# Kernel optimization log

Measured on AMD Instinct MI355X. Metric: run time of the kernel, lower is better.

Reference implementation:

```python
import jax, jax.numpy as jnp
import numpy as np

D, H, HD, FF, L, SYM, B = 256, 8, 32, 256, 3, 64, 32768


def setup_inputs() -> dict:
    key = jax.random.key(0)
    ks = iter(jax.random.split(key, 32))
    n = lambda shape, s=0.02: jax.random.normal(next(ks), shape, dtype=jnp.float32) * s
    return {
        "global_emb": n((B, D), 1.0),
        "pert_emb": n((B, D), 1.0),
        "sym_feat": n((B, SYM), 1.0),
        "ppi_feat": n((B, D), 1.0),
        "sym_W": n((SYM, D)),
        "sym_b": jnp.zeros((D,), jnp.float32),
        "sym_ln_g": jnp.ones((D,), jnp.float32),
        "sym_ln_b": jnp.zeros((D,), jnp.float32),
        "token_type_emb": n((4, D)),
        "Wqkv": n((L, D, 3 * D)),
        "bqkv": jnp.zeros((L, 3 * D), jnp.float32),
        "Wo": n((L, D, D)),
        "bo": jnp.zeros((L, D), jnp.float32),
        "ln1_g": jnp.ones((L, D), jnp.float32),
        "ln1_b": jnp.zeros((L, D), jnp.float32),
        "ln2_g": jnp.ones((L, D), jnp.float32),
        "ln2_b": jnp.zeros((L, D), jnp.float32),
        "W1": n((L, D, FF)),
        "b1": jnp.zeros((L, FF), jnp.float32),
        "W2": n((L, FF, D)),
        "b2": jnp.zeros((L, D), jnp.float32),
        "final_ln_g": jnp.ones((D,), jnp.float32),
        "final_ln_b": jnp.zeros((D,), jnp.float32),
        "out_ln_g": jnp.ones((D,), jnp.float32),
        "out_ln_b": jnp.zeros((D,), jnp.float32),
    }


def _ln(x, g, b, eps=1e-5):
    m = jnp.mean(x, axis=-1, keepdims=True)
    v = jnp.mean(jnp.square(x - m), axis=-1, keepdims=True)
    return (x - m) * jax.lax.rsqrt(v + eps) * g + b


def reference(global_emb, pert_emb, sym_feat, ppi_feat, sym_W, sym_b, sym_ln_g,
              sym_ln_b, token_type_emb, Wqkv, bqkv, Wo, bo, ln1_g, ln1_b,
              ln2_g, ln2_b, W1, b1, W2, b2, final_ln_g, final_ln_b,
              out_ln_g, out_ln_b):
    # sym projection + LN, then stack 4 tokens and add token-type embedding
    sym_proj = _ln(sym_feat @ sym_W + sym_b, sym_ln_g, sym_ln_b)
    x = jnp.stack([global_emb, pert_emb, sym_proj, ppi_feat], axis=1)  # [B,4,D]
    x = x + token_type_emb[None]
    Bsz = x.shape[0]
    scale = 1.0 / np.sqrt(HD).astype(np.float32)
    for l in range(L):  # pre-norm TransformerEncoderLayer x3 (eval: dropout off)
        h = _ln(x, ln1_g[l], ln1_b[l])
        qkv = h @ Wqkv[l] + bqkv[l]  # [B,4,3D]
        q, k, v = jnp.split(qkv, 3, axis=-1)
        q = q.reshape(Bsz, 4, H, HD).transpose(0, 2, 1, 3)  # [B,H,4,HD]
        k = k.reshape(Bsz, 4, H, HD).transpose(0, 2, 1, 3)
        v = v.reshape(Bsz, 4, H, HD).transpose(0, 2, 1, 3)
        attn = jax.nn.softmax(jnp.einsum("bhqd,bhkd->bhqk", q, k) * scale, axis=-1)
        o = jnp.einsum("bhqk,bhkd->bhqd", attn, v)
        o = o.transpose(0, 2, 1, 3).reshape(Bsz, 4, D)
        x = x + (o @ Wo[l] + bo[l])
        h2 = _ln(x, ln2_g[l], ln2_b[l])
        ff = jax.nn.gelu(h2 @ W1[l] + b1[l], approximate=False) @ W2[l] + b2[l]
        x = x + ff
    x = _ln(x, final_ln_g, final_ln_b)  # TransformerEncoder final norm
    return _ln(jnp.mean(x, axis=1), out_ln_g, out_ln_b)  # mean over 4 tokens + out_norm
```

## Files before the change

kernel.cpp:

```cpp
#include <hip/hip_runtime.h>
#include <hip/hip_bf16.h>
#include <math.h>

typedef unsigned short u16;
typedef __attribute__((ext_vector_type(8))) short v8s;
typedef __attribute__((ext_vector_type(4))) short v4s;
typedef __attribute__((ext_vector_type(4))) float v4f;

__device__ __forceinline__ float bf2f(u16 u){
  union { float f; unsigned int i; } v; v.i = ((unsigned int)u) << 16; return v.f;
}
__device__ __forceinline__ u16 f2bf(float f){
  union { __hip_bfloat16 h; u16 u; } cv; cv.h = __float2bfloat16(f); return cv.u;
}
__device__ __forceinline__ bool det_bf16(const void* p){
  return ((const u16*)p)[0] != 0;
}
__device__ __forceinline__ float ldp(const void* p, size_t i, bool bf){
  return bf ? bf2f(((const u16*)p)[i]) : ((const float*)p)[i];
}
__device__ __forceinline__ void ld8f(const void* p, size_t i, bool bf, float* o){
  if (bf){
    v8s a = *(const v8s*)((const u16*)p + i);
    #pragma unroll
    for (int j=0;j<8;j++) o[j]=bf2f((u16)a[j]);
  } else {
    const float4* q=(const float4*)((const float*)p + i);
    float4 a=q[0], b=q[1];
    o[0]=a.x;o[1]=a.y;o[2]=a.z;o[3]=a.w;o[4]=b.x;o[5]=b.y;o[6]=b.z;o[7]=b.w;
  }
}
__device__ __forceinline__ void ld4f(const void* p, size_t i, bool bf, float* o){
  if (bf){
    v4s a = *(const v4s*)((const u16*)p + i);
    #pragma unroll
    for (int j=0;j<4;j++) o[j]=bf2f((u16)a[j]);
  } else {
    float4 q = *(const float4*)((const float*)p + i);
    o[0]=q.x;o[1]=q.y;o[2]=q.z;o[3]=q.w;
  }
}

#define MFMA(a,b,c) __builtin_amdgcn_mfma_f32_16x16x32_bf16((a),(b),(c),0,0,0)

template<int CTRL>
__device__ __forceinline__ float dpp_qp(float x){
  union { float f; int i; } u; u.f = x;
  u.i = __builtin_amdgcn_mov_dpp(u.i, CTRL, 0xF, 0xF, true);
  return u.f;
}

__device__ __forceinline__ int swz(int row, int col, int stride){
  return row*stride + ((((col>>3) ^ (row&7))<<3) | (col&7));
}

__device__ __forceinline__ void st4(u16* dst, v4f a, const float* b){
  v4s o;
  #pragma unroll
  for (int i=0;i<4;i++) o[i] = (short)f2bf(a[i] + b[i]);
  *(v4s*)dst = o;
}
__device__ __forceinline__ void rmw4(u16* p, v4f a, const float* b){
  v4s x = *(v4s*)p; v4s o;
  #pragma unroll
  for (int i=0;i<4;i++) o[i] = (short)f2bf(bf2f((u16)x[i]) + a[i] + b[i]);
  *(v4s*)p = o;
}

__device__ __forceinline__ float gelu_f(float u){
  float ax = fabsf(u)*0.70710678118f;
  float t = 1.f/(1.f + 0.3275911f*ax);
  float y = t*(0.254829592f + t*(-0.284496736f + t*(1.421413741f +
            t*(-1.453152027f + t*1.061405429f))));
  float er = 1.f - y*__expf(-ax*ax);
  er = copysignf(er, u);
  return 0.5f*u*(1.f + er);
}

__global__ __launch_bounds__(64) void repack_kernel(
    const void* __restrict__ symW, const void* __restrict__ Wqkv,
    const void* __restrict__ Wo, const void* __restrict__ W1, const void* __restrict__ W2,
    u16* __restrict__ wf_sym, u16* __restrict__ wf_qkv, u16* __restrict__ wf_o,
    u16* __restrict__ wf_1, u16* __restrict__ wf_2, const void* __restrict__ dtp)
{
  bool bf = det_bf16(dtp);
  int idx = blockIdx.x;
  const void* src; u16* dst; int N, kb, nb; size_t soff;
  if (idx < 32) { src = symW; dst = wf_sym; N = 256; kb = idx >> 4; nb = idx & 15; soff = 0; }
  else {
    idx -= 32;
    int lay = idx / 768, r = idx % 768;
    if (r < 384) { N = 768; src = Wqkv; soff = (size_t)lay*196608; dst = wf_qkv + lay*196608; kb = r/48; nb = r%48; }
    else {
      r -= 384; int which = r >> 7, rr = r & 127; N = 256; kb = rr >> 4; nb = rr & 15;
      soff = (size_t)lay*65536;
      if (which == 0)      { src = Wo; dst = wf_o + lay*65536; }
      else if (which == 1) { src = W1; dst = wf_1 + lay*65536; }
      else                 { src = W2; dst = wf_2 + lay*65536; }
    }
  }
  int ln = threadIdx.x;
  int n  = nb*16 + (ln & 15);
  int k0 = kb*32 + (ln >> 4)*8;
  u16* d = dst + (((size_t)(kb*(N>>4) + nb))*64 + ln)*8;
  #pragma unroll
  for (int j = 0; j < 8; j++) d[j] = f2bf(ldp(src, soff + (size_t)(k0+j)*N + n, bf));
}

__device__ __forceinline__ void ln64s(const u16* src, u16* dst,
    const void* gp, const void* bp, size_t goff, bool bf, int t)
{
  int r = t>>3, p = t&7;
  float vv[32];
  float su=0.f, sq=0.f;
  #pragma unroll
  for (int k4=0;k4<4;k4++){
    v8s a = *(const v8s*)(src + swz(r, p*32+k4*8, 256));
    #pragma unroll
    for (int j=0;j<8;j++){ float v=bf2f((u16)a[j]); vv[k4*8+j]=v; su+=v; sq+=v*v; }
  }
  su += dpp_qp<0xB1>(su); sq += dpp_qp<0xB1>(sq);
  su += dpp_qp<0x4E>(su); sq += dpp_qp<0x4E>(sq);
  su += __shfl_xor(su,4); sq += __shfl_xor(sq,4);
  float m = su*(1.f/256.f);
  float rs = rsqrtf(sq*(1.f/256.f) - m*m + 1e-5f);
  #pragma unroll
  for (int k4=0;k4<4;k4++){
    float gg[8], bb[8];
    ld8f(gp, goff + p*32 + k4*8, bf, gg);
    ld8f(bp, goff + p*32 + k4*8, bf, bb);
    v8s o;
    #pragma unroll
    for (int j=0;j<8;j++) o[j]=(short)f2bf((vv[k4*8+j]-m)*rs*gg[j]+bb[j]);
    *(v8s*)(dst + swz(r, p*32+k4*8, 256)) = o;
  }
}

__global__ __launch_bounds__(512,4) void fused_kernel(
    const void* __restrict__ gemb, const void* __restrict__ pemb,
    const void* __restrict__ symf, const void* __restrict__ ppi,
    const void* __restrict__ symb, const void* __restrict__ slng,
    const void* __restrict__ slnb, const void* __restrict__ tte,
    const void* __restrict__ bqkv, const void* __restrict__ bo,
    const void* __restrict__ ln1g, const void* __restrict__ ln1b,
    const void* __restrict__ ln2g, const void* __restrict__ ln2b,
    const void* __restrict__ b1p, const void* __restrict__ b2p,
    const void* __restrict__ flng, const void* __restrict__ flnb,
    const void* __restrict__ olng, const void* __restrict__ olnb,
    const u16* __restrict__ wf_sym, const u16* __restrict__ wf_qkv,
    const u16* __restrict__ wf_o, const u16* __restrict__ wf_1,
    const u16* __restrict__ wf_2,
    void* __restrict__ out)
{
  __shared__ __align__(16) u16 X[16384];
  __shared__ __align__(16) u16 H[16384];
  __shared__ __align__(16) u16 symst[1024];

  bool bf = det_bf16(slng);
  int t = threadIdx.x;
  int w = t>>6, ln = t&63, quad = ln>>4, c = ln&15;
  int row0 = blockIdx.x * 64;
  int S0 = row0 >> 2;

  {
    if (t < 128){
      int r = t>>3, pp = t&7;
      float tmp[8];
      ld8f(symf, (size_t)(S0+r)*64 + pp*8, bf, tmp);
      v8s o;
      #pragma unroll
      for (int j=0;j<8;j++) o[j]=(short)f2bf(tmp[j]);
      *(v8s*)(symst + swz(r, pp*8, 64)) = o;
    } else {
      int u = t-128;
      int rid = u>>3, p = u&7;
      int s = rid/3, z = rid - s*3;
      int tok = (z==2)?3:z;
      const void* src = (z==0)?gemb: (z==1)?pemb: ppi;
      #pragma unroll
      for (int k4=0;k4<4;k4++){
        float a8[8], t8[8];
        ld8f(src, (size_t)(S0+s)*256 + p*32 + k4*8, bf, a8);
        ld8f(tte, (size_t)tok*256 + p*32 + k4*8, bf, t8);
        v8s o;
        #pragma unroll
        for (int j=0;j<8;j++) o[j]=(short)f2bf(a8[j]+t8[j]);
        *(v8s*)(X + swz(s*4+tok, p*32+k4*8, 256)) = o;
      }
    }
    __syncthreads();
    {
      v4f acc[2];
      v4f z4={0.f,0.f,0.f,0.f};
      acc[0]=z4; acc[1]=z4;
      #pragma unroll
      for (int kb=0;kb<2;kb++){
        v8s a = *(const v8s*)(symst + swz(c, kb*32+quad*8, 64));
        #pragma unroll
        for (int j=0;j<2;j++){
          v8s b = *(const v8s*)(wf_sym + (((size_t)(kb*16+w*2+j))*64+ln)*8);
          acc[j] = MFMA(b, a, acc[j]);
        }
      }
      #pragma unroll
      for (int j=0;j<2;j++){
        int colb = (w*2+j)*16 + quad*4;
        float sb[4]; ld4f(symb, colb, bf, sb);
        st4(H + swz(c, colb, 256), acc[j], sb);
      }
    }
    __syncthreads();
    if (t < 128){
      int r = t>>3, p = t&7;
      float vv[32];
      float su=0.f, sq=0.f;
      #pragma unroll
      for (int k4=0;k4<4;k4++){
        v8s a = *(const v8s*)(H + swz(r, p*32+k4*8, 256));
        #pragma unroll
        for (int j=0;j<8;j++){ float v=bf2f((u16)a[j]); vv[k4*8+j]=v; su+=v; sq+=v*v; }
      }
      su += dpp_qp<0xB1>(su); sq += dpp_qp<0xB1>(sq);
      su += dpp_qp<0x4E>(su); sq += dpp_qp<0x4E>(sq);
      su += __shfl_xor(su,4); sq += __shfl_xor(sq,4);
      float m = su*(1.f/256.f);
      float rs = rsqrtf(sq*(1.f/256.f) - m*m + 1e-5f);
      #pragma unroll
      for (int k4=0;k4<4;k4++){
        float gg[8], bb[8], t8[8];
        ld8f(slng, p*32+k4*8, bf, gg);
        ld8f(slnb, p*32+k4*8, bf, bb);
        ld8f(tte, 512 + p*32+k4*8, bf, t8);
        v8s o;
        #pragma unroll
        for (int j=0;j<8;j++) o[j]=(short)f2bf((vv[k4*8+j]-m)*rs*gg[j]+bb[j]+t8[j]);
        *(v8s*)(X + swz(r*4+2, p*32+k4*8, 256)) = o;
      }
    }
    __syncthreads();
  }

  #pragma unroll 1
  for (int lay = 0; lay < 3; lay++){

    ln64s(X, H, ln1g, ln1b, (size_t)lay*256, bf, t);
    __syncthreads();

    {
      const u16* wq = wf_qkv + (size_t)lay*196608;
      int h = w;
      v4f z4={0.f,0.f,0.f,0.f};
      const float scl = 0.17677669529663687f;
      v4f p01[2], p23[2];
      auto qkhalf = [&](int hf, v4f* pout){
        v4f Qa[2][2], Ka[2][2];
        #pragma unroll
        for (int m2=0;m2<2;m2++){ Qa[m2][0]=z4;Qa[m2][1]=z4;Ka[m2][0]=z4;Ka[m2][1]=z4; }
        #pragma unroll 2
        for (int kb=0;kb<8;kb++){
          v8s Bq0 = *(const v8s*)(wq + (((size_t)(kb*48      + h*2  ))*64+ln)*8);
          v8s Bq1 = *(const v8s*)(wq + (((size_t)(kb*48      + h*2+1))*64+ln)*8);
          v8s Bk0 = *(const v8s*)(wq + (((size_t)(kb*48 + 16 + h*2  ))*64+ln)*8);
          v8s Bk1 = *(const v8s*)(wq + (((size_t)(kb*48 + 16 + h*2+1))*64+ln)*8);
          #pragma unroll
          for (int m2=0;m2<2;m2++){
            v8s a = *(const v8s*)(H + swz((hf*2+m2)*16+c, kb*32+quad*8, 256));
            Qa[m2][0]=MFMA(Bq0,a,Qa[m2][0]);
            Qa[m2][1]=MFMA(Bq1,a,Qa[m2][1]);
            Ka[m2][0]=MFMA(Bk0,a,Ka[m2][0]);
            Ka[m2][1]=MFMA(Bk1,a,Ka[m2][1]);
          }
        }
        float bq2[2][4], bk2[2][4];
        #pragma unroll
        for (int jj=0;jj<2;jj++){
          ld4f(bqkv, (size_t)lay*768 +       h*32 + jj*16 + quad*4, bf, bq2[jj]);
          ld4f(bqkv, (size_t)lay*768 + 256 + h*32 + jj*16 + quad*4, bf, bk2[jj]);
        }
        #pragma unroll
        for (int m2=0;m2<2;m2++){
          float q8[8], k8[8];
          #pragma unroll
          for (int jj=0;jj<2;jj++)
            #pragma unroll
            for (int i=0;i<4;i++){
              q8[jj*4+i] = Qa[m2][jj][i] + bq2[jj][i];
              k8[jj*4+i] = Ka[m2][jj][i] + bk2[jj][i];
            }
          float sp0=0.f, sp1=0.f, sp2=0.f, sp3=0.f;
          #pragma unroll
          for (int x=0;x<8;x++){
            sp0 += q8[x]*k8[x];
            sp1 += q8[x]*dpp_qp<0xB1>(k8[x]);
            sp2 += q8[x]*dpp_qp<0x4E>(k8[x]);
            sp3 += q8[x]*dpp_qp<0x1B>(k8[x]);
          }
          sp0 += __shfl_xor(sp0,16); sp0 += __shfl_xor(sp0,32);
          sp1 += __shfl_xor(sp1,16); sp1 += __shfl_xor(sp1,32);
          sp2 += __shfl_xor(sp2,16); sp2 += __shfl_xor(sp2,32);
          sp3 += __shfl_xor(sp3,16); sp3 += __shfl_xor(sp3,32);
          float s0=sp0*scl, s1=sp1*scl, s2=sp2*scl, s3=sp3*scl;
          float mx = fmaxf(fmaxf(s0,s1),fmaxf(s2,s3));
          float e0=__expf(s0-mx), e1=__expf(s1-mx), e2=__expf(s2-mx), e3=__expf(s3-mx);
          float inv = 1.f/(e0+e1+e2+e3);
          v4f p; p[0]=e0*inv; p[1]=e1*inv; p[2]=e2*inv; p[3]=e3*inv;
          pout[m2] = p;
        }
      };
      qkhalf(0, p01);
      __builtin_amdgcn_sched_barrier(0);
      qkhalf(1, p23);
      v4f Va[4][2];
      #pragma unroll
      for (int mb=0;mb<4;mb++){ Va[mb][0]=z4; Va[mb][1]=z4; }
      #pragma unroll 2
      for (int kb=0;kb<8;kb++){
        v8s Bv0 = *(const v8s*)(wq + (((size_t)(kb*48 + 32 + h*2  ))*64+ln)*8);
        v8s Bv1 = *(const v8s*)(wq + (((size_t)(kb*48 + 32 + h*2+1))*64+ln)*8);
        #pragma unroll
        for (int mb=0;mb<4;mb++){
          v8s a = *(const v8s*)(H + swz(mb*16+c, kb*32+quad*8, 256));
          Va[mb][0]=MFMA(Bv0,a,Va[mb][0]);
          Va[mb][1]=MFMA(Bv1,a,Va[mb][1]);
        }
      }
      __syncthreads();
      float bv[2][4];
      #pragma unroll
      for (int jj=0;jj<2;jj++)
        ld4f(bqkv, (size_t)lay*768 + 512 + h*32 + jj*16 + quad*4, bf, bv[jj]);
      #pragma unroll
      for (int mb=0;mb<4;mb++){
        v4f P = (mb==0)?p01[0]:(mb==1)?p01[1]:(mb==2)?p23[0]:p23[1];
        #pragma unroll
        for (int jj=0;jj<2;jj++){
          v4f o;
          #pragma unroll
          for (int i=0;i<4;i++){
            float v = Va[mb][jj][i] + bv[jj][i];
            float r = P[0]*v;
            r += P[1]*dpp_qp<0xB1>(v);
            r += P[2]*dpp_qp<0x4E>(v);
            r += P[3]*dpp_qp<0x1B>(v);
            o[i] = r;
          }
          v4s pk;
          #pragma unroll
          for (int i=0;i<4;i++) pk[i]=(short)f2bf(o[i]);
          *(v4s*)(H + swz(mb*16+c, h*32 + jj*16 + quad*4, 256)) = pk;
        }
      }
    }
    __syncthreads();

    {
      const u16* wo = wf_o + (size_t)lay*65536;
      v4f acc[4][2];
      v4f z4={0.f,0.f,0.f,0.f};
      #pragma unroll
      for (int mb=0;mb<4;mb++){ acc[mb][0]=z4; acc[mb][1]=z4; }
      #pragma unroll 2
      for (int kb=0;kb<8;kb++){
        v8s B0 = *(const v8s*)(wo + (((size_t)(kb*16 + w*2  ))*64+ln)*8);
        v8s B1 = *(const v8s*)(wo + (((size_t)(kb*16 + w*2+1))*64+ln)*8);
        #pragma unroll
        for (int mb=0;mb<4;mb++){
          v8s a = *(const v8s*)(H + swz(mb*16+c, kb*32+quad*8, 256));
          acc[mb][0]=MFMA(B0,a,acc[mb][0]);
          acc[mb][1]=MFMA(B1,a,acc[mb][1]);
        }
      }
      #pragma unroll
      for (int jj=0;jj<2;jj++){
        int colb = (w*2+jj)*16 + quad*4;
        float bs[4]; ld4f(bo, (size_t)lay*256 + colb, bf, bs);
        #pragma unroll
        for (int mb=0;mb<4;mb++)
          rmw4(X + swz(mb*16+c, colb, 256), acc[mb][jj], bs);
      }
    }
    __syncthreads();

    ln64s(X, H, ln2g, ln2b, (size_t)lay*256, bf, t);
    __syncthreads();

    {
      const u16* w1 = wf_1 + (size_t)lay*65536;
      v4f acc[4][2];
      v4f z4={0.f,0.f,0.f,0.f};
      #pragma unroll
      for (int mb=0;mb<4;mb++){ acc[mb][0]=z4; acc[mb][1]=z4; }
      #pragma unroll 2
      for (int kb=0;kb<8;kb++){
        v8s B0 = *(const v8s*)(w1 + (((size_t)(kb*16 + w*2  ))*64+ln)*8);
        v8s B1 = *(const v8s*)(w1 + (((size_t)(kb*16 + w*2+1))*64+ln)*8);
        #pragma unroll
        for (int mb=0;mb<4;mb++){
          v8s a = *(const v8s*)(H + swz(mb*16+c, kb*32+quad*8, 256));
          acc[mb][0]=MFMA(B0,a,acc[mb][0]);
          acc[mb][1]=MFMA(B1,a,acc[mb][1]);
        }
      }
      __syncthreads();
      #pragma unroll
      for (int jj=0;jj<2;jj++){
        int colb = (w*2+jj)*16 + quad*4;
        float bs[4]; ld4f(b1p, (size_t)lay*256 + colb, bf, bs);
        #pragma unroll
        for (int mb=0;mb<4;mb++){
          v4s pk;
          #pragma unroll
          for (int i=0;i<4;i++) pk[i]=(short)f2bf(gelu_f(acc[mb][jj][i] + bs[i]));
          *(v4s*)(H + swz(mb*16+c, colb, 256)) = pk;
        }
      }
    }
    __syncthreads();

    {
      const u16* w2 = wf_2 + (size_t)lay*65536;
      v4f acc[4][2];
      v4f z4={0.f,0.f,0.f,0.f};
      #pragma unroll
      for (int mb=0;mb<4;mb++){ acc[mb][0]=z4; acc[mb][1]=z4; }
      #pragma unroll 2
      for (int kb=0;kb<8;kb++){
        v8s B0 = *(const v8s*)(w2 + (((size_t)(kb*16 + w*2  ))*64+ln)*8);
        v8s B1 = *(const v8s*)(w2 + (((size_t)(kb*16 + w*2+1))*64+ln)*8);
        #pragma unroll
        for (int mb=0;mb<4;mb++){
          v8s a = *(const v8s*)(H + swz(mb*16+c, kb*32+quad*8, 256));
          acc[mb][0]=MFMA(B0,a,acc[mb][0]);
          acc[mb][1]=MFMA(B1,a,acc[mb][1]);
        }
      }
      #pragma unroll
      for (int jj=0;jj<2;jj++){
        int colb = (w*2+jj)*16 + quad*4;
        float bs[4]; ld4f(b2p, (size_t)lay*256 + colb, bf, bs);
        #pragma unroll
        for (int mb=0;mb<4;mb++)
          rmw4(X + swz(mb*16+c, colb, 256), acc[mb][jj], bs);
      }
    }
    __syncthreads();
  }

  ln64s(X, H, flng, flnb, 0, bf, t);
  __syncthreads();
  if (t < 128){
    int s = t>>3, p = t&7;
    float y[32];
    #pragma unroll
    for (int j=0;j<32;j++) y[j]=0.f;
    #pragma unroll
    for (int r4=0;r4<4;r4++)
      #pragma unroll
      for (int k4=0;k4<4;k4++){
        v8s a = *(const v8s*)(H + swz(s*4+r4, p*32+k4*8, 256));
        #pragma unroll
        for (int j=0;j<8;j++) y[k4*8+j] += bf2f((u16)a[j]);
      }
    float su=0.f, sq=0.f;
    #pragma unroll
    for (int j=0;j<32;j++){ y[j]*=0.25f; su+=y[j]; sq+=y[j]*y[j]; }
    su += dpp_qp<0xB1>(su); sq += dpp_qp<0xB1>(sq);
    su += dpp_qp<0x4E>(su); sq += dpp_qp<0x4E>(sq);
    su += __shfl_xor(su,4); sq += __shfl_xor(sq,4);
    float m = su*(1.f/256.f);
    float rs = rsqrtf(sq*(1.f/256.f) - m*m + 1e-5f);
    #pragma unroll
    for (int k4=0;k4<4;k4++){
      float gg[8], bb[8];
      ld8f(olng, p*32+k4*8, bf, gg);
      ld8f(olnb, p*32+k4*8, bf, bb);
      if (bf){
        u16* dst = (u16*)out + (size_t)(S0+s)*256 + p*32 + k4*8;
        v8s o;
        #pragma unroll
        for (int j=0;j<8;j++) o[j]=(short)f2bf((y[k4*8+j]-m)*rs*gg[j]+bb[j]);
        *(v8s*)dst = o;
      } else {
        float* dst = (float*)out + (size_t)(S0+s)*256 + p*32 + k4*8;
        #pragma unroll
        for (int j=0;j<8;j++) dst[j] = (y[k4*8+j]-m)*rs*gg[j]+bb[j];
      }
    }
  }
}

extern "C" void kernel_launch(void* const* d_in, const int* in_sizes, int n_in,
                              void* d_out, int out_size, void* d_ws, size_t ws_size,
                              hipStream_t stream)
{
  const void* gemb=d_in[0];
  const void* pemb=d_in[1];
  const void* symf=d_in[2];
  const void* ppi =d_in[3];
  const void* symW=d_in[4];
  const void* symb=d_in[5];
  const void* slng=d_in[6];
  const void* slnb=d_in[7];
  const void* tte =d_in[8];
  const void* Wqkv=d_in[9];
  const void* bqkv=d_in[10];
  const void* Wo  =d_in[11];
  const void* bo  =d_in[12];
  const void* ln1g=d_in[13];
  const void* ln1b=d_in[14];
  const void* ln2g=d_in[15];
  const void* ln2b=d_in[16];
  const void* W1  =d_in[17];
  const void* b1  =d_in[18];
  const void* W2  =d_in[19];
  const void* b2  =d_in[20];
  const void* flng=d_in[21];
  const void* flnb=d_in[22];
  const void* olng=d_in[23];
  const void* olnb=d_in[24];

  u16* wf_sym=(u16*)d_ws;
  u16* wf_qkv=wf_sym + 16384;
  u16* wf_o  =wf_qkv + 589824;
  u16* wf_1  =wf_o  + 196608;
  u16* wf_2  =wf_1  + 196608;

  repack_kernel<<<2336,64,0,stream>>>(symW,Wqkv,Wo,W1,W2, wf_sym,wf_qkv,wf_o,wf_1,wf_2, slng);
  fused_kernel<<<2048,512,0,stream>>>(
      gemb,pemb,symf,ppi,symb,slng,slnb,tte,bqkv,bo,
      ln1g,ln1b,ln2g,ln2b,b1,b2,flng,flnb,olng,olnb,
      wf_sym,wf_qkv,wf_o,wf_1,wf_2, d_out);
}
```

Before: 772.9 us.

## Fold pre-norm LayerNorm into QKV and FFN1 weights via post-GEMM correction

Instead of materialising LayerNorm outputs into shared memory before the QKV and W1 GEMMs, the gamma scale is folded into the repacked weights. The GEMMs then run directly on the raw residual X, and the result is corrected per row using the mean and rstd plus precomputed column sums of gamma*W and beta*W+bias. This removes a full LN write pass and a barrier per norm, and lets the softmax and V epilogues absorb the correction. In exchange it adds extra repack blocks and per-row stat reads. Numerics change because bf16 GEMMs now run on unnormalised inputs, and mean subtraction after the GEMM can lose precision.

```diff
diff --git a/kernel.cpp b/kernel.cpp
--- a/kernel.cpp
+++ b/kernel.cpp
@@ -80,31 +80,67 @@
 __global__ __launch_bounds__(64) void repack_kernel(
     const void* __restrict__ symW, const void* __restrict__ Wqkv,
     const void* __restrict__ Wo, const void* __restrict__ W1, const void* __restrict__ W2,
+    const void* __restrict__ ln1g, const void* __restrict__ ln1b,
+    const void* __restrict__ ln2g, const void* __restrict__ ln2b,
+    const void* __restrict__ bqkv, const void* __restrict__ b1,
     u16* __restrict__ wf_sym, u16* __restrict__ wf_qkv, u16* __restrict__ wf_o,
-    u16* __restrict__ wf_1, u16* __restrict__ wf_2, const void* __restrict__ dtp)
+    u16* __restrict__ wf_1, u16* __restrict__ wf_2,
+    float* __restrict__ cq1, float* __restrict__ cq0,
+    float* __restrict__ cf1, float* __restrict__ cf0,
+    const void* __restrict__ dtp)
 {
   bool bf = det_bf16(dtp);
   int idx = blockIdx.x;
+  int ln = threadIdx.x;
+
+  if (idx >= 2336){
+    int i2 = idx - 2336;
+    int lay = i2 >> 4, r2 = i2 & 15;
+    const void *Wp, *g, *be, *bb; size_t woff, goff, boff; int N, n; float *o1, *o0;
+    if (r2 < 12){
+      n = r2*64 + ln; N = 768; Wp = Wqkv; woff = (size_t)lay*196608;
+      g = ln1g; be = ln1b; bb = bqkv; goff = (size_t)lay*256; boff = (size_t)lay*768;
+      o1 = cq1 + lay*768; o0 = cq0 + lay*768;
+    } else {
+      int rr = r2 - 12; n = rr*64 + ln; N = 256; Wp = W1; woff = (size_t)lay*65536;
+      g = ln2g; be = ln2b; bb = b1; goff = (size_t)lay*256; boff = (size_t)lay*256;
+      o1 = cf1 + lay*256; o0 = cf0 + lay*256;
+    }
+    float a1 = 0.f, a0 = 0.f;
+    for (int k = 0; k < 256; k++){
+      float wv = ldp(Wp, woff + (size_t)k*N + n, bf);
+      a1 += bf2f(f2bf(ldp(g, goff+k, bf) * wv));
+      a0 += ldp(be, goff+k, bf) * wv;
+    }
+    o1[n] = a1;
+    o0[n] = a0 + ldp(bb, boff + n, bf);
+    return;
+  }
+
   const void* src; u16* dst; int N, kb, nb; size_t soff;
+  const void* gscale = nullptr; size_t gsoff = 0;
   if (idx < 32) { src = symW; dst = wf_sym; N = 256; kb = idx >> 4; nb = idx & 15; soff = 0; }
   else {
     idx -= 32;
     int lay = idx / 768, r = idx % 768;
-    if (r < 384) { N = 768; src = Wqkv; soff = (size_t)lay*196608; dst = wf_qkv + lay*196608; kb = r/48; nb = r%48; }
+    if (r < 384) { N = 768; src = Wqkv; soff = (size_t)lay*196608; dst = wf_qkv + lay*196608; kb = r/48; nb = r%48;
+                   gscale = ln1g; gsoff = (size_t)lay*256; }
     else {
       r -= 384; int which = r >> 7, rr = r & 127; N = 256; kb = rr >> 4; nb = rr & 15;
       soff = (size_t)lay*65536;
       if (which == 0)      { src = Wo; dst = wf_o + lay*65536; }
-      else if (which == 1) { src = W1; dst = wf_1 + lay*65536; }
+      else if (which == 1) { src = W1; dst = wf_1 + lay*65536; gscale = ln2g; gsoff = (size_t)lay*256; }
       else                 { src = W2; dst = wf_2 + lay*65536; }
     }
   }
-  int ln = threadIdx.x;
   int n  = nb*16 + (ln & 15);
   int k0 = kb*32 + (ln >> 4)*8;
   u16* d = dst + (((size_t)(kb*(N>>4) + nb))*64 + ln)*8;
   #pragma unroll
-  for (int j = 0; j < 8; j++) d[j] = f2bf(ldp(src, soff + (size_t)(k0+j)*N + n, bf));
+  for (int j = 0; j < 8; j++){
+    float sc = gscale ? ldp(gscale, gsoff + k0 + j, bf) : 1.f;
+    d[j] = f2bf(sc * ldp(src, soff + (size_t)(k0+j)*N + n, bf));
+  }
 }
 
 __device__ __forceinline__ void ln64s(const u16* src, u16* dst,
@@ -136,17 +172,33 @@
   }
 }
 
+__device__ __forceinline__ void mrs64(const u16* src, float* dst, int t){
+  int r = t>>3, p = t&7;
+  float su=0.f, sq=0.f;
+  #pragma unroll
+  for (int k4=0;k4<4;k4++){
+    v8s a = *(const v8s*)(src + swz(r, p*32+k4*8, 256));
+    #pragma unroll
+    for (int j=0;j<8;j++){ float v=bf2f((u16)a[j]); su+=v; sq+=v*v; }
+  }
+  su += dpp_qp<0xB1>(su); sq += dpp_qp<0xB1>(sq);
+  su += dpp_qp<0x4E>(su); sq += dpp_qp<0x4E>(sq);
+  su += __shfl_xor(su,4); sq += __shfl_xor(sq,4);
+  float m = su*(1.f/256.f);
+  float rs = rsqrtf(sq*(1.f/256.f) - m*m + 1e-5f);
+  if (p == 0){ dst[2*r] = m; dst[2*r+1] = rs; }
+}
+
 __global__ __launch_bounds__(512,4) void fused_kernel(
     const void* __restrict__ gemb, const void* __restrict__ pemb,
     const void* __restrict__ symf, const void* __restrict__ ppi,
     const void* __restrict__ symb, const void* __restrict__ slng,
     const void* __restrict__ slnb, const void* __restrict__ tte,
-    const void* __restrict__ bqkv, const void* __restrict__ bo,
-    const void* __restrict__ ln1g, const void* __restrict__ ln1b,
-    const void* __restrict__ ln2g, const void* __restrict__ ln2b,
-    const void* __restrict__ b1p, const void* __restrict__ b2p,
+    const void* __restrict__ bo, const void* __restrict__ b2p,
     const void* __restrict__ flng, const void* __restrict__ flnb,
     const void* __restrict__ olng, const void* __restrict__ olnb,
+    const float* __restrict__ cq1, const float* __restrict__ cq0,
+    const float* __restrict__ cf1, const float* __restrict__ cf0,
     const u16* __restrict__ wf_sym, const u16* __restrict__ wf_qkv,
     const u16* __restrict__ wf_o, const u16* __restrict__ wf_1,
     const u16* __restrict__ wf_2,
@@ -155,6 +207,8 @@
   __shared__ __align__(16) u16 X[16384];
   __shared__ __align__(16) u16 H[16384];
   __shared__ __align__(16) u16 symst[1024];
+  __shared__ __align__(8)  float mrsA[128];
+  __shared__ __align__(8)  float mrsB[128];
 
   bool bf = det_bf16(slng);
   int t = threadIdx.x;
@@ -243,16 +297,15 @@
   #pragma unroll 1
   for (int lay = 0; lay < 3; lay++){
 
-    ln64s(X, H, ln1g, ln1b, (size_t)lay*256, bf, t);
-    __syncthreads();
+    mrs64(X, mrsA, t);
 
     {
       const u16* wq = wf_qkv + (size_t)lay*196608;
       int h = w;
       v4f z4={0.f,0.f,0.f,0.f};
       const float scl = 0.17677669529663687f;
-      v4f p01[2], p23[2];
-      auto qkhalf = [&](int hf, v4f* pout){
+      v4f s01[2], s23[2];
+      auto qkdots = [&](int hf, v4f* sout){
         v4f Qa[2][2], Ka[2][2];
         #pragma unroll
         for (int m2=0;m2<2;m2++){ Qa[m2][0]=z4;Qa[m2][1]=z4;Ka[m2][0]=z4;Ka[m2][1]=z4; }
@@ -264,28 +317,33 @@
           v8s Bk1 = *(const v8s*)(wq + (((size_t)(kb*48 + 16 + h*2+1))*64+ln)*8);
           #pragma unroll
           for (int m2=0;m2<2;m2++){
-            v8s a = *(const v8s*)(H + swz((hf*2+m2)*16+c, kb*32+quad*8, 256));
+            v8s a = *(const v8s*)(X + swz((hf*2+m2)*16+c, kb*32+quad*8, 256));
             Qa[m2][0]=MFMA(Bq0,a,Qa[m2][0]);
             Qa[m2][1]=MFMA(Bq1,a,Qa[m2][1]);
             Ka[m2][0]=MFMA(Bk0,a,Ka[m2][0]);
             Ka[m2][1]=MFMA(Bk1,a,Ka[m2][1]);
           }
         }
-        float bq2[2][4], bk2[2][4];
+        if (hf == 0) __syncthreads();
+        v4f q1[2], q0[2], k1[2], k0f[2];
         #pragma unroll
         for (int jj=0;jj<2;jj++){
-          ld4f(bqkv, (size_t)lay*768 +       h*32 + jj*16 + quad*4, bf, bq2[jj]);
-          ld4f(bqkv, (size_t)lay*768 + 256 + h*32 + jj*16 + quad*4, bf, bk2[jj]);
+          int d0 = lay*768 + h*32 + jj*16 + quad*4;
+          q1[jj]  = *(const v4f*)(cq1 + d0);
+          q0[jj]  = *(const v4f*)(cq0 + d0);
+          k1[jj]  = *(const v4f*)(cq1 + d0 + 256);
+          k0f[jj] = *(const v4f*)(cq0 + d0 + 256);
         }
         #pragma unroll
         for (int m2=0;m2<2;m2++){
+          float2 mr = *(const float2*)&mrsA[2*((hf*2+m2)*16 + c)];
           float q8[8], k8[8];
           #pragma unroll
           for (int jj=0;jj<2;jj++)
             #pragma unroll
             for (int i=0;i<4;i++){
-              q8[jj*4+i] = Qa[m2][jj][i] + bq2[jj][i];
-              k8[jj*4+i] = Ka[m2][jj][i] + bk2[jj][i];
+              q8[jj*4+i] = mr.y*(Qa[m2][jj][i] - mr.x*q1[jj][i]) + q0[jj][i];
+              k8[jj*4+i] = mr.y*(Ka[m2][jj][i] - mr.x*k1[jj][i]) + k0f[jj][i];
             }
           float sp0=0.f, sp1=0.f, sp2=0.f, sp3=0.f;
           #pragma unroll
@@ -299,17 +357,24 @@
           sp1 += __shfl_xor(sp1,16); sp1 += __shfl_xor(sp1,32);
           sp2 += __shfl_xor(sp2,16); sp2 += __shfl_xor(sp2,32);
           sp3 += __shfl_xor(sp3,16); sp3 += __shfl_xor(sp3,32);
-          float s0=sp0*scl, s1=sp1*scl, s2=sp2*scl, s3=sp3*scl;
-          float mx = fmaxf(fmaxf(s0,s1),fmaxf(s2,s3));
-          float e0=__expf(s0-mx), e1=__expf(s1-mx), e2=__expf(s2-mx), e3=__expf(s3-mx);
+          v4f s; s[0]=sp0*scl; s[1]=sp1*scl; s[2]=sp2*scl; s[3]=sp3*scl;
+          sout[m2] = s;
+        }
+      };
+      qkdots(0, s01);
+      __builtin_amdgcn_sched_barrier(0);
+      qkdots(1, s23);
+      v4f p0, p1, p2, p3;
+      {
+        auto smax = [&](v4f s)->v4f{
+          float mx = fmaxf(fmaxf(s[0],s[1]),fmaxf(s[2],s[3]));
+          float e0=__expf(s[0]-mx), e1=__expf(s[1]-mx), e2=__expf(s[2]-mx), e3=__expf(s[3]-mx);
           float inv = 1.f/(e0+e1+e2+e3);
           v4f p; p[0]=e0*inv; p[1]=e1*inv; p[2]=e2*inv; p[3]=e3*inv;
-          pout[m2] = p;
-        }
-      };
-      qkhalf(0, p01);
-      __builtin_amdgcn_sched_barrier(0);
-      qkhalf(1, p23);
+          return p;
+        };
+        p0 = smax(s01[0]); p1 = smax(s01[1]); p2 = smax(s23[0]); p3 = smax(s23[1]);
+      }
       v4f Va[4][2];
       #pragma unroll
       for (int mb=0;mb<4;mb++){ Va[mb][0]=z4; Va[mb][1]=z4; }
@@ -319,25 +384,38 @@
         v8s Bv1 = *(const v8s*)(wq + (((size_t)(kb*48 + 32 + h*2+1))*64+ln)*8);
         #pragma unroll
         for (int mb=0;mb<4;mb++){
-          v8s a = *(const v8s*)(H + swz(mb*16+c, kb*32+quad*8, 256));
+          v8s a = *(const v8s*)(X + swz(mb*16+c, kb*32+quad*8, 256));
           Va[mb][0]=MFMA(Bv0,a,Va[mb][0]);
           Va[mb][1]=MFMA(Bv1,a,Va[mb][1]);
         }
       }
-      __syncthreads();
-      float bv[2][4];
-      #pragma unroll
-      for (int jj=0;jj<2;jj++)
-        ld4f(bqkv, (size_t)lay*768 + 512 + h*32 + jj*16 + quad*4, bf, bv[jj]);
+      {
+        v4f v1[2], v0[2];
+        #pragma unroll
+        for (int jj=0;jj<2;jj++){
+          int d0 = lay*768 + 512 + h*32 + jj*16 + quad*4;
+          v1[jj] = *(const v4f*)(cq1 + d0);
+          v0[jj] = *(const v4f*)(cq0 + d0);
+        }
+        #pragma unroll
+        for (int mb=0;mb<4;mb++){
+          float2 mr = *(const float2*)&mrsA[2*(mb*16 + c)];
+          #pragma unroll
+          for (int jj=0;jj<2;jj++)
+            #pragma unroll
+            for (int i=0;i<4;i++)
+              Va[mb][jj][i] = mr.y*(Va[mb][jj][i] - mr.x*v1[jj][i]) + v0[jj][i];
+        }
+      }
       #pragma unroll
       for (int mb=0;mb<4;mb++){
-        v4f P = (mb==0)?p01[0]:(mb==1)?p01[1]:(mb==2)?p23[0]:p23[1];
+        v4f P = (mb==0)?p0:(mb==1)?p1:(mb==2)?p2:p3;
         #pragma unroll
         for (int jj=0;jj<2;jj++){
           v4f o;
           #pragma unroll
           for (int i=0;i<4;i++){
-            float v = Va[mb][jj][i] + bv[jj][i];
+            float v = Va[mb][jj][i];
             float r = P[0]*v;
             r += P[1]*dpp_qp<0xB1>(v);
             r += P[2]*dpp_qp<0x4E>(v);
@@ -381,8 +459,7 @@
     }
     __syncthreads();
 
-    ln64s(X, H, ln2g, ln2b, (size_t)lay*256, bf, t);
-    __syncthreads();
+    mrs64(X, mrsB, t);
 
     {
       const u16* w1 = wf_1 + (size_t)lay*65536;
@@ -396,7 +473,7 @@
         v8s B1 = *(const v8s*)(w1 + (((size_t)(kb*16 + w*2+1))*64+ln)*8);
         #pragma unroll
         for (int mb=0;mb<4;mb++){
-          v8s a = *(const v8s*)(H + swz(mb*16+c, kb*32+quad*8, 256));
+          v8s a = *(const v8s*)(X + swz(mb*16+c, kb*32+quad*8, 256));
           acc[mb][0]=MFMA(B0,a,acc[mb][0]);
           acc[mb][1]=MFMA(B1,a,acc[mb][1]);
         }
@@ -405,12 +482,17 @@
       #pragma unroll
       for (int jj=0;jj<2;jj++){
         int colb = (w*2+jj)*16 + quad*4;
-        float bs[4]; ld4f(b1p, (size_t)lay*256 + colb, bf, bs);
+        v4f f1 = *(const v4f*)(cf1 + lay*256 + colb);
+        v4f f0 = *(const v4f*)(cf0 + lay*256 + colb);
         #pragma unroll
         for (int mb=0;mb<4;mb++){
+          float2 mr = *(const float2*)&mrsB[2*(mb*16 + c)];
           v4s pk;
           #pragma unroll
-          for (int i=0;i<4;i++) pk[i]=(short)f2bf(gelu_f(acc[mb][jj][i] + bs[i]));
+          for (int i=0;i<4;i++){
+            float val = mr.y*(acc[mb][jj][i] - mr.x*f1[i]) + f0[i];
+            pk[i]=(short)f2bf(gelu_f(val));
+          }
           *(v4s*)(H + swz(mb*16+c, colb, 256)) = pk;
         }
       }
@@ -524,10 +606,16 @@
   u16* wf_o  =wf_qkv + 589824;
   u16* wf_1  =wf_o  + 196608;
   u16* wf_2  =wf_1  + 196608;
-
-  repack_kernel<<<2336,64,0,stream>>>(symW,Wqkv,Wo,W1,W2, wf_sym,wf_qkv,wf_o,wf_1,wf_2, slng);
+  float* cq1 = (float*)(wf_2 + 196608);
+  float* cq0 = cq1 + 2304;
+  float* cf1 = cq0 + 2304;
+  float* cf0 = cf1 + 768;
+
+  repack_kernel<<<2384,64,0,stream>>>(symW,Wqkv,Wo,W1,W2,
+      ln1g,ln1b,ln2g,ln2b,bqkv,b1,
+      wf_sym,wf_qkv,wf_o,wf_1,wf_2, cq1,cq0,cf1,cf0, slng);
   fused_kernel<<<2048,512,0,stream>>>(
-      gemb,pemb,symf,ppi,symb,slng,slnb,tte,bqkv,bo,
-      ln1g,ln1b,ln2g,ln2b,b1,b2,flng,flnb,olng,olnb,
+      gemb,pemb,symf,ppi,symb,slng,slnb,tte,bo,b2,
+      flng,flnb,olng,olnb, cq1,cq0,cf1,cf0,
       wf_sym,wf_qkv,wf_o,wf_1,wf_2, d_out);
 }
```

After: 727.8 us. 5.8% less time.
